# Kernel tuning notes

Hardware: AMD Instinct MI355X
Metric: run time of the kernel (lower is better)

Reference implementation:

```python
import jax, jax.numpy as jnp
import numpy as np

NEG_INF = -1e10  # matches torch's -10000000000.0 fill


def setup_inputs() -> dict:
    key = jax.random.key(0)
    k1, k2, k3, k4, k5, k6 = jax.random.split(key, 6)
    B, N, D_IN, D_HID, D_OUT = 8, 2048, 512, 512, 512
    H = jax.random.normal(k1, (B, N, D_IN), dtype=jnp.float32)
    bias = jax.random.normal(k2, (B, N, N), dtype=jnp.float32)
    mask = jax.random.randint(k3, (B, N, N), 0, 2, dtype=jnp.int32)
    s = 1.0 / np.sqrt(D_IN)
    Wq = jax.random.normal(k4, (D_IN, D_HID), dtype=jnp.float32) * s
    Wk = jax.random.normal(k5, (D_IN, D_HID), dtype=jnp.float32) * s
    Wv = jax.random.normal(k6, (D_IN, D_OUT), dtype=jnp.float32) * s
    return {"H": H, "bias": bias, "mask": mask, "Wq": Wq, "Wk": Wk, "Wv": Wv}


def reference(H, bias, mask, Wq, Wk, Wv):
    # Q,K: [B,N,d_hid], V: [B,N,d_out]
    Q = H @ Wq
    K = H @ Wk
    V = H @ Wv
    d = Q.shape[-1]
    scale = 1.0 / jnp.sqrt(jnp.asarray(d, dtype=Q.dtype))
    # scores: [B,N,N]; scale, add bias, then fill masked-out entries
    scores = jnp.einsum("bnd,bmd->bnm", Q, K) * scale + bias
    scores = jnp.where(mask == 0, jnp.asarray(NEG_INF, scores.dtype), scores)
    atn = jax.nn.softmax(scores, axis=-1)
    return jnp.einsum("bnm,bmo->bno", atn, V)
```

## Files before the change

kernel.cpp:

```cpp
#include <hip/hip_runtime.h>
#include <hip/hip_bf16.h>

typedef __attribute__((ext_vector_type(8))) short short8;
typedef __attribute__((ext_vector_type(4))) float floatx4;

#define NB 8
#define NN 2048
#define DD 512

__device__ __forceinline__ unsigned short f2bf(float f) {
  union { float f; unsigned int u; } v; v.f = f;
  unsigned int u = v.u;
  return (unsigned short)((u + 0x7fffu + ((u >> 16) & 1u)) >> 16);
}
__device__ __forceinline__ float bf2f(unsigned short s) {
  union { unsigned int u; float f; } v; v.u = ((unsigned int)s) << 16;
  return v.f;
}

typedef __attribute__((address_space(3))) unsigned short lds_us;
typedef __attribute__((address_space(1))) const unsigned short glb_us;

__device__ __forceinline__ void ld_lds16(const unsigned short* g, unsigned short* l) {
  __builtin_amdgcn_global_load_lds((glb_us*)g, (lds_us*)l, 16, 0, 0);
}

__global__ __launch_bounds__(256) void mha_cvtH(const float* __restrict__ H,
                                                unsigned short* __restrict__ Hb, int n8) {
  int i = blockIdx.x * 256 + threadIdx.x;
  if (i >= n8) return;
  const float4* src = (const float4*)H;
  float4 a = src[2 * i], b = src[2 * i + 1];
  short8 o;
  o[0] = (short)f2bf(a.x); o[1] = (short)f2bf(a.y); o[2] = (short)f2bf(a.z); o[3] = (short)f2bf(a.w);
  o[4] = (short)f2bf(b.x); o[5] = (short)f2bf(b.y); o[6] = (short)f2bf(b.z); o[7] = (short)f2bf(b.w);
  *(short8*)(Hb + 8 * i) = o;
}

__global__ __launch_bounds__(256) void mha_tW(const float* __restrict__ Wq, const float* __restrict__ Wk,
                                              const float* __restrict__ Wv,
                                              unsigned short* __restrict__ Wqt, unsigned short* __restrict__ Wkt,
                                              unsigned short* __restrict__ Wvt) {
  const float* W = (blockIdx.z == 0) ? Wq : (blockIdx.z == 1) ? Wk : Wv;
  unsigned short* Wt = (blockIdx.z == 0) ? Wqt : (blockIdx.z == 1) ? Wkt : Wvt;
  __shared__ float tile[32][33];
  int d0 = blockIdx.x * 32, k0 = blockIdx.y * 32;
  int t = threadIdx.x, r = t >> 3, c4 = (t & 7) * 4;
  float4 v = *(const float4*)(W + (size_t)(k0 + r) * DD + d0 + c4);
  tile[r][c4] = v.x; tile[r][c4 + 1] = v.y; tile[r][c4 + 2] = v.z; tile[r][c4 + 3] = v.w;
  __syncthreads();
  union { unsigned short s[4]; uint2 v; } u;
  u.s[0] = f2bf(tile[c4][r]);     u.s[1] = f2bf(tile[c4 + 1][r]);
  u.s[2] = f2bf(tile[c4 + 2][r]); u.s[3] = f2bf(tile[c4 + 3][r]);
  *(uint2*)(Wt + (size_t)(d0 + r) * DD + k0 + c4) = u.v;
}

__global__ __launch_bounds__(256) void mha_tV(const unsigned short* __restrict__ Vr,
                                              unsigned short* __restrict__ Vt) {
  int b = blockIdx.z;
  int d0 = blockIdx.x * 32, n0 = blockIdx.y * 32;
  __shared__ unsigned short tile[32][34];
  int t = threadIdx.x, r = t >> 3, c4 = (t & 7) * 4;
  union { uint2 v; unsigned short s[4]; } u;
  u.v = *(const uint2*)(Vr + ((size_t)b * NN + n0 + r) * DD + d0 + c4);
  tile[r][c4] = u.s[0]; tile[r][c4 + 1] = u.s[1]; tile[r][c4 + 2] = u.s[2]; tile[r][c4 + 3] = u.s[3];
  __syncthreads();
  union { unsigned short s[4]; uint2 v; } o;
  o.s[0] = tile[c4][r]; o.s[1] = tile[c4 + 1][r]; o.s[2] = tile[c4 + 2][r]; o.s[3] = tile[c4 + 3][r];
  *(uint2*)(Vt + ((size_t)b * DD + d0 + r) * NN + n0 + c4) = o.v;
}


__device__ __forceinline__ void stage_tile_async(const unsigned short* __restrict__ g, int ld,
                                                 unsigned short* s, int t) {
#pragma unroll
  for (int h = 0; h < 2; ++h) {
    int c = t + h * 256;
    int r = c >> 2, p = c & 3;
    int seg = (p - (r >> 1)) & 3;
    ld_lds16(g + (size_t)r * ld + seg * 8, s + c * 8);
  }
}

__device__ __forceinline__ void mfma_step(const unsigned short* As, const unsigned short* Bs,
                                          int wr, int wc, int quad, int lr, floatx4 acc[4][4]) {
  short8 a[4], b[4];
#pragma unroll
  for (int i = 0; i < 4; ++i) {
    int ra = wr * 64 + i * 16 + lr;
    int rb = wc * 64 + i * 16 + lr;
    a[i] = *(const short8*)(As + ra * 32 + ((quad + (ra >> 1)) & 3) * 8);
    b[i] = *(const short8*)(Bs + rb * 32 + ((quad + (rb >> 1)) & 3) * 8);
  }
#pragma unroll
  for (int i = 0; i < 4; ++i)
#pragma unroll
    for (int j = 0; j < 4; ++j)
      acc[i][j] = __builtin_amdgcn_mfma_f32_16x16x32_bf16(a[i], b[j], acc[i][j], 0, 0, 0);
}

__global__ __launch_bounds__(256) void mha_proj(const unsigned short* __restrict__ Hb,
                                                const unsigned short* __restrict__ Wqt,
                                                const unsigned short* __restrict__ Wkt,
                                                const unsigned short* __restrict__ Wvt,
                                                unsigned short* __restrict__ Qb,
                                                unsigned short* __restrict__ Kb,
                                                unsigned short* __restrict__ Vr) {
  const unsigned short* Wt = (blockIdx.z == 0) ? Wqt : (blockIdx.z == 1) ? Wkt : Wvt;
  unsigned short* dst = (blockIdx.z == 0) ? Qb : (blockIdx.z == 1) ? Kb : Vr;
  __shared__ unsigned short As[128 * 32], Bs[128 * 32];
  int t = threadIdx.x, wave = t >> 6, lane = t & 63, quad = lane >> 4, lr = lane & 15;
  int wr = wave >> 1, wc = wave & 1;
  int m0 = blockIdx.y * 128, n0 = blockIdx.x * 128;
  floatx4 acc[4][4] = {};
  for (int k0 = 0; k0 < DD; k0 += 32) {
    __syncthreads();
    stage_tile_async(Hb + (size_t)m0 * DD + k0, DD, As, t);
    stage_tile_async(Wt + (size_t)n0 * DD + k0, DD, Bs, t);
    __syncthreads();
    mfma_step(As, Bs, wr, wc, quad, lr, acc);
  }
#pragma unroll
  for (int i = 0; i < 4; ++i)
#pragma unroll
    for (int j = 0; j < 4; ++j)
#pragma unroll
      for (int r = 0; r < 4; ++r) {
        int row = m0 + wr * 64 + i * 16 + quad * 4 + r;
        int col = n0 + wc * 64 + j * 16 + lr;
        dst[(size_t)row * DD + col] = f2bf(acc[i][j][r]);
      }
}

__global__ __launch_bounds__(256) void mha_scores(const unsigned short* __restrict__ Qb,
                                                  const unsigned short* __restrict__ Kb,
                                                  const float* __restrict__ bias,
                                                  const int* __restrict__ mask,
                                                  unsigned short* __restrict__ E,
                                                  float* __restrict__ l) {
  int b = blockIdx.z;
  int i0 = blockIdx.y * 128;
  int j0 = blockIdx.x * 128;
  __shared__ unsigned short As[128 * 32], Bs[128 * 32];
  int t = threadIdx.x, wave = t >> 6, lane = t & 63, quad = lane >> 4, lr = lane & 15;
  int wr = wave >> 1, wc = wave & 1;
  const unsigned short* Q = Qb + (size_t)b * NN * DD;
  const unsigned short* K = Kb + (size_t)b * NN * DD;
  const float scale = 0.04419417382415922f;

  floatx4 acc[4][4] = {};
  for (int k0 = 0; k0 < DD; k0 += 32) {
    __syncthreads();
    stage_tile_async(Q + (size_t)i0 * DD + k0, DD, As, t);
    stage_tile_async(K + (size_t)j0 * DD + k0, DD, Bs, t);
    __syncthreads();
    mfma_step(As, Bs, wr, wc, quad, lr, acc);
  }

  float rs[4][4] = {};
#pragma unroll
  for (int i = 0; i < 4; ++i) {
    int row = i0 + wr * 64 + i * 16 + quad * 4;
#pragma unroll
    for (int j = 0; j < 4; ++j) {
      int col = j0 + wc * 64 + j * 16 + lr;
      size_t base = ((size_t)b * NN + row) * NN + col;
#pragma unroll
      for (int r = 0; r < 4; ++r) {
        size_t off = base + (size_t)r * NN;
        float bi = __builtin_nontemporal_load(&bias[off]);
        int mk = __builtin_nontemporal_load(&mask[off]);
        float s = acc[i][j][r] * scale + bi - 16.0f;
        float e = (mk != 0) ? __expf(s) : 0.0f;
        unsigned short eb = f2bf(e);
        E[off] = eb;
        rs[i][r] += bf2f(eb);
      }
    }
  }
#pragma unroll
  for (int i = 0; i < 4; ++i)
#pragma unroll
    for (int r = 0; r < 4; ++r) {
      float v = rs[i][r];
      v += __shfl_xor(v, 1);
      v += __shfl_xor(v, 2);
      v += __shfl_xor(v, 4);
      v += __shfl_xor(v, 8);
      if (lr == 0) {
        int row = i0 + wr * 64 + i * 16 + quad * 4 + r;
        atomicAdd(&l[b * NN + row], v);
      }
    }
}

__global__ __launch_bounds__(256) void mha_pv(const unsigned short* __restrict__ E,
                                              const unsigned short* __restrict__ Vt,
                                              const float* __restrict__ l,
                                              float* __restrict__ out) {
  int b = blockIdx.z;
  int i0 = blockIdx.y * 128;
  int c0 = blockIdx.x * 128;
  __shared__ unsigned short As[128 * 32], Bs[128 * 32];
  int t = threadIdx.x, wave = t >> 6, lane = t & 63, quad = lane >> 4, lr = lane & 15;
  int wr = wave >> 1, wc = wave & 1;
  const unsigned short* Eb = E + (size_t)b * NN * NN;
  const unsigned short* Vb = Vt + (size_t)b * DD * NN;
  floatx4 acc[4][4] = {};
  for (int k0 = 0; k0 < NN; k0 += 32) {
    __syncthreads();
    stage_tile_async(Eb + (size_t)i0 * NN + k0, NN, As, t);
    stage_tile_async(Vb + (size_t)c0 * NN + k0, NN, Bs, t);
    __syncthreads();
    mfma_step(As, Bs, wr, wc, quad, lr, acc);
  }
#pragma unroll
  for (int i = 0; i < 4; ++i)
#pragma unroll
    for (int r = 0; r < 4; ++r) {
      int row = i0 + wr * 64 + i * 16 + quad * 4 + r;
      float linv = 1.0f / l[b * NN + row];
#pragma unroll
      for (int j = 0; j < 4; ++j) {
        int col = c0 + wc * 64 + j * 16 + lr;
        __builtin_nontemporal_store(acc[i][j][r] * linv,
                                    &out[((size_t)b * NN + row) * DD + col]);
      }
    }
}

extern "C" void kernel_launch(void* const* d_in, const int* in_sizes, int n_in,
                              void* d_out, int out_size, void* d_ws, size_t ws_size,
                              hipStream_t stream) {
  const float* H = (const float*)d_in[0];
  const float* bias = (const float*)d_in[1];
  const int* mask = (const int*)d_in[2];
  const float* Wq = (const float*)d_in[3];
  const float* Wk = (const float*)d_in[4];
  const float* Wv = (const float*)d_in[5];
  float* out = (float*)d_out;
  char* ws = (char*)d_ws;

  const size_t SZ_QKV = (size_t)NB * NN * DD * 2;
  const size_t SZ_W = (size_t)DD * DD * 2;
  unsigned short* Qb = (unsigned short*)(ws);
  unsigned short* Kb = (unsigned short*)(ws + SZ_QKV);
  unsigned short* Vt = (unsigned short*)(ws + 2 * SZ_QKV);
  float* l = (float*)(ws + 3 * SZ_QKV);
  char* base2 = ws + 3 * SZ_QKV + (((size_t)NB * NN * 4 + 255) & ~255ULL);
  unsigned short* E = (unsigned short*)(base2);
  unsigned short* Hb = (unsigned short*)(base2);
  unsigned short* Wqt = (unsigned short*)(base2 + SZ_QKV);
  unsigned short* Wkt = (unsigned short*)(base2 + SZ_QKV + SZ_W);
  unsigned short* Wvt = (unsigned short*)(base2 + SZ_QKV + 2 * SZ_W);
  unsigned short* Vr = (unsigned short*)(base2 + SZ_QKV + 3 * SZ_W);

  hipMemsetAsync(l, 0, (size_t)NB * NN * 4, stream);
  mha_cvtH<<<dim3((NB * NN * DD / 8) / 256), 256, 0, stream>>>(H, Hb, NB * NN * DD / 8);
  mha_tW<<<dim3(DD / 32, DD / 32, 3), 256, 0, stream>>>(Wq, Wk, Wv, Wqt, Wkt, Wvt);
  mha_proj<<<dim3(DD / 128, NB * NN / 128, 3), 256, 0, stream>>>(Hb, Wqt, Wkt, Wvt, Qb, Kb, Vr);
  mha_tV<<<dim3(DD / 32, NN / 32, NB), 256, 0, stream>>>(Vr, Vt);
  mha_scores<<<dim3(NN / 128, NN / 128, NB), 256, 0, stream>>>(Qb, Kb, bias, mask, E, l);
  mha_pv<<<dim3(DD / 128, NN / 128, NB), 256, 0, stream>>>(E, Vt, l, out);
}
```

Before: 587.4 us.

## Fuse score and PV kernels into flash-style attention without materialized E

Replaces the separate scores kernel (which wrote a bf16 exp-score matrix E to global memory) and the PV kernel with one fused kernel. Each block handles 32 query rows for one batch, loops over key tiles, builds exp scores in LDS, and multiplies them by V directly. Row sums are reduced in shared memory, which removes the global atomics and the memset. This avoids writing and reading back the large E matrix. The cost is that each block now reloads K and V for every 32-row tile, and the tiles are smaller with fewer blocks (8x64).

```diff
diff --git a/kernel.cpp b/kernel.cpp
--- a/kernel.cpp
+++ b/kernel.cpp
@@ -132,100 +132,143 @@
       }
 }
 
-__global__ __launch_bounds__(256) void mha_scores(const unsigned short* __restrict__ Qb,
-                                                  const unsigned short* __restrict__ Kb,
-                                                  const float* __restrict__ bias,
-                                                  const int* __restrict__ mask,
-                                                  unsigned short* __restrict__ E,
-                                                  float* __restrict__ l) {
-  int b = blockIdx.z;
-  int i0 = blockIdx.y * 128;
-  int j0 = blockIdx.x * 128;
-  __shared__ unsigned short As[128 * 32], Bs[128 * 32];
+__global__ __launch_bounds__(256, 2) void mha_fused(const unsigned short* __restrict__ Qb,
+                                                    const unsigned short* __restrict__ Kb,
+                                                    const unsigned short* __restrict__ Vt,
+                                                    const float* __restrict__ bias,
+                                                    const int* __restrict__ mask,
+                                                    float* __restrict__ out) {
+  __shared__ unsigned short smem[40960];
+  unsigned short* Qs = smem;
+  unsigned short* Ks = smem + 4096;
+  unsigned short* Ps = smem + 20480;
+  unsigned short* Vs = smem + 24576;
+  float* ls = (float*)smem;
+
+  int b = blockIdx.x;
+  int i0 = blockIdx.y * 32;
   int t = threadIdx.x, wave = t >> 6, lane = t & 63, quad = lane >> 4, lr = lane & 15;
-  int wr = wave >> 1, wc = wave & 1;
-  const unsigned short* Q = Qb + (size_t)b * NN * DD;
-  const unsigned short* K = Kb + (size_t)b * NN * DD;
+  const unsigned short* Qg = Qb + ((size_t)b * NN + i0) * DD;
+  const unsigned short* Kg = Kb + (size_t)b * NN * DD;
+  const unsigned short* Vg = Vt + (size_t)b * DD * NN;
   const float scale = 0.04419417382415922f;
 
-  floatx4 acc[4][4] = {};
-  for (int k0 = 0; k0 < DD; k0 += 32) {
+  floatx4 acc[2][8] = {};
+  float rs[2][4] = {};
+
+  for (int jt = 0; jt < 16; ++jt) {
+    int j0 = jt * 128;
+    floatx4 sacc[2][2] = {};
+
+    for (int k0 = 0; k0 < DD; k0 += 128) {
+      __syncthreads();
+#pragma unroll
+      for (int h = 0; h < 2; ++h) {
+        int d = t + h * 256;
+        int s = d >> 7, w = d & 127, r = w >> 2, p = w & 3;
+        int l = (p - (r >> 1)) & 3;
+        ld_lds16(Qg + (size_t)r * DD + k0 + (s * 4 + l) * 8, Qs + d * 8);
+      }
+#pragma unroll
+      for (int h = 0; h < 8; ++h) {
+        int d = t + h * 256;
+        int s = d >> 9, w = d & 511, r = w >> 2, p = w & 3;
+        int l = (p - (r >> 1)) & 3;
+        ld_lds16(Kg + (size_t)(j0 + r) * DD + k0 + (s * 4 + l) * 8, Ks + d * 8);
+      }
+      __syncthreads();
+#pragma unroll
+      for (int ss = 0; ss < 4; ++ss) {
+        short8 a[2], bb[2];
+#pragma unroll
+        for (int i = 0; i < 2; ++i) {
+          int ra = i * 16 + lr;
+          a[i] = *(const short8*)(Qs + ss * 1024 + ra * 32 + ((quad + (ra >> 1)) & 3) * 8);
+        }
+#pragma unroll
+        for (int j = 0; j < 2; ++j) {
+          int rb = wave * 32 + j * 16 + lr;
+          bb[j] = *(const short8*)(Ks + ss * 4096 + rb * 32 + ((quad + (rb >> 1)) & 3) * 8);
+        }
+#pragma unroll
+        for (int i = 0; i < 2; ++i)
+#pragma unroll
+          for (int j = 0; j < 2; ++j)
+            sacc[i][j] = __builtin_amdgcn_mfma_f32_16x16x32_bf16(a[i], bb[j], sacc[i][j], 0, 0, 0);
+      }
+    }
+
+#pragma unroll
+    for (int i = 0; i < 2; ++i)
+#pragma unroll
+      for (int jj = 0; jj < 2; ++jj)
+#pragma unroll
+        for (int rr = 0; rr < 4; ++rr) {
+          int row_l = i * 16 + quad * 4 + rr;
+          int jloc = jj * 16 + lr;
+          size_t off = ((size_t)b * NN + i0 + row_l) * NN + (j0 + wave * 32 + jloc);
+          float bi = __builtin_nontemporal_load(&bias[off]);
+          int mk = __builtin_nontemporal_load(&mask[off]);
+          float s = sacc[i][jj][rr] * scale + bi - 16.0f;
+          float e = (mk != 0) ? __expf(s) : 0.0f;
+          unsigned short eb = f2bf(e);
+          Ps[wave * 1024 + row_l * 32 + (((jloc >> 3) + (row_l >> 1)) & 3) * 8 + (jloc & 7)] = eb;
+          rs[i][rr] += bf2f(eb);
+        }
     __syncthreads();
-    stage_tile_async(Q + (size_t)i0 * DD + k0, DD, As, t);
-    stage_tile_async(K + (size_t)j0 * DD + k0, DD, Bs, t);
-    __syncthreads();
-    mfma_step(As, Bs, wr, wc, quad, lr, acc);
-  }
-
-  float rs[4][4] = {};
-#pragma unroll
-  for (int i = 0; i < 4; ++i) {
-    int row = i0 + wr * 64 + i * 16 + quad * 4;
-#pragma unroll
-    for (int j = 0; j < 4; ++j) {
-      int col = j0 + wc * 64 + j * 16 + lr;
-      size_t base = ((size_t)b * NN + row) * NN + col;
-#pragma unroll
-      for (int r = 0; r < 4; ++r) {
-        size_t off = base + (size_t)r * NN;
-        float bi = __builtin_nontemporal_load(&bias[off]);
-        int mk = __builtin_nontemporal_load(&mask[off]);
-        float s = acc[i][j][r] * scale + bi - 16.0f;
-        float e = (mk != 0) ? __expf(s) : 0.0f;
-        unsigned short eb = f2bf(e);
-        E[off] = eb;
-        rs[i][r] += bf2f(eb);
+
+    for (int jk = 0; jk < 4; ++jk) {
+      if (jk) __syncthreads();
+#pragma unroll
+      for (int h = 0; h < 8; ++h) {
+        int d = t + h * 256;
+        int r = d >> 2, p = d & 3;
+        int l = (p - (r >> 1)) & 3;
+        ld_lds16(Vg + (size_t)r * NN + j0 + jk * 32 + l * 8, Vs + d * 8);
+      }
+      __syncthreads();
+      short8 a[2];
+#pragma unroll
+      for (int i = 0; i < 2; ++i) {
+        int ra = i * 16 + lr;
+        a[i] = *(const short8*)(Ps + jk * 1024 + ra * 32 + ((quad + (ra >> 1)) & 3) * 8);
+      }
+#pragma unroll
+      for (int jc = 0; jc < 8; ++jc) {
+        int rb = wave * 128 + jc * 16 + lr;
+        short8 bv = *(const short8*)(Vs + rb * 32 + ((quad + (rb >> 1)) & 3) * 8);
+        acc[0][jc] = __builtin_amdgcn_mfma_f32_16x16x32_bf16(a[0], bv, acc[0][jc], 0, 0, 0);
+        acc[1][jc] = __builtin_amdgcn_mfma_f32_16x16x32_bf16(a[1], bv, acc[1][jc], 0, 0, 0);
       }
     }
   }
-#pragma unroll
-  for (int i = 0; i < 4; ++i)
-#pragma unroll
-    for (int r = 0; r < 4; ++r) {
-      float v = rs[i][r];
+
+  __syncthreads();
+  if (t < 32) ls[t] = 0.0f;
+  __syncthreads();
+#pragma unroll
+  for (int i = 0; i < 2; ++i)
+#pragma unroll
+    for (int rr = 0; rr < 4; ++rr) {
+      float v = rs[i][rr];
       v += __shfl_xor(v, 1);
       v += __shfl_xor(v, 2);
       v += __shfl_xor(v, 4);
       v += __shfl_xor(v, 8);
-      if (lr == 0) {
-        int row = i0 + wr * 64 + i * 16 + quad * 4 + r;
-        atomicAdd(&l[b * NN + row], v);
-      }
+      if (lr == 0) atomicAdd(&ls[i * 16 + quad * 4 + rr], v);
     }
-}
-
-__global__ __launch_bounds__(256) void mha_pv(const unsigned short* __restrict__ E,
-                                              const unsigned short* __restrict__ Vt,
-                                              const float* __restrict__ l,
-                                              float* __restrict__ out) {
-  int b = blockIdx.z;
-  int i0 = blockIdx.y * 128;
-  int c0 = blockIdx.x * 128;
-  __shared__ unsigned short As[128 * 32], Bs[128 * 32];
-  int t = threadIdx.x, wave = t >> 6, lane = t & 63, quad = lane >> 4, lr = lane & 15;
-  int wr = wave >> 1, wc = wave & 1;
-  const unsigned short* Eb = E + (size_t)b * NN * NN;
-  const unsigned short* Vb = Vt + (size_t)b * DD * NN;
-  floatx4 acc[4][4] = {};
-  for (int k0 = 0; k0 < NN; k0 += 32) {
-    __syncthreads();
-    stage_tile_async(Eb + (size_t)i0 * NN + k0, NN, As, t);
-    stage_tile_async(Vb + (size_t)c0 * NN + k0, NN, Bs, t);
-    __syncthreads();
-    mfma_step(As, Bs, wr, wc, quad, lr, acc);
-  }
-#pragma unroll
-  for (int i = 0; i < 4; ++i)
-#pragma unroll
-    for (int r = 0; r < 4; ++r) {
-      int row = i0 + wr * 64 + i * 16 + quad * 4 + r;
-      float linv = 1.0f / l[b * NN + row];
-#pragma unroll
-      for (int j = 0; j < 4; ++j) {
-        int col = c0 + wc * 64 + j * 16 + lr;
-        __builtin_nontemporal_store(acc[i][j][r] * linv,
-                                    &out[((size_t)b * NN + row) * DD + col]);
-      }
+  __syncthreads();
+
+#pragma unroll
+  for (int i = 0; i < 2; ++i)
+#pragma unroll
+    for (int rr = 0; rr < 4; ++rr) {
+      int row_l = i * 16 + quad * 4 + rr;
+      float linv = 1.0f / ls[row_l];
+      size_t rowoff = ((size_t)b * NN + i0 + row_l) * DD + wave * 128;
+#pragma unroll
+      for (int jc = 0; jc < 8; ++jc)
+        __builtin_nontemporal_store(acc[i][jc][rr] * linv, &out[rowoff + jc * 16 + lr]);
     }
 }
 
@@ -246,20 +289,15 @@
   unsigned short* Qb = (unsigned short*)(ws);
   unsigned short* Kb = (unsigned short*)(ws + SZ_QKV);
   unsigned short* Vt = (unsigned short*)(ws + 2 * SZ_QKV);
-  float* l = (float*)(ws + 3 * SZ_QKV);
-  char* base2 = ws + 3 * SZ_QKV + (((size_t)NB * NN * 4 + 255) & ~255ULL);
-  unsigned short* E = (unsigned short*)(base2);
-  unsigned short* Hb = (unsigned short*)(base2);
-  unsigned short* Wqt = (unsigned short*)(base2 + SZ_QKV);
-  unsigned short* Wkt = (unsigned short*)(base2 + SZ_QKV + SZ_W);
-  unsigned short* Wvt = (unsigned short*)(base2 + SZ_QKV + 2 * SZ_W);
-  unsigned short* Vr = (unsigned short*)(base2 + SZ_QKV + 3 * SZ_W);
-
-  hipMemsetAsync(l, 0, (size_t)NB * NN * 4, stream);
+  unsigned short* Hb = (unsigned short*)(ws + 3 * SZ_QKV);
+  unsigned short* Wqt = (unsigned short*)(ws + 4 * SZ_QKV);
+  unsigned short* Wkt = (unsigned short*)(ws + 4 * SZ_QKV + SZ_W);
+  unsigned short* Wvt = (unsigned short*)(ws + 4 * SZ_QKV + 2 * SZ_W);
+  unsigned short* Vr = (unsigned short*)(ws + 4 * SZ_QKV + 3 * SZ_W);
+
   mha_cvtH<<<dim3((NB * NN * DD / 8) / 256), 256, 0, stream>>>(H, Hb, NB * NN * DD / 8);
   mha_tW<<<dim3(DD / 32, DD / 32, 3), 256, 0, stream>>>(Wq, Wk, Wv, Wqt, Wkt, Wvt);
   mha_proj<<<dim3(DD / 128, NB * NN / 128, 3), 256, 0, stream>>>(Hb, Wqt, Wkt, Wvt, Qb, Kb, Vr);
   mha_tV<<<dim3(DD / 32, NN / 32, NB), 256, 0, stream>>>(Vr, Vt);
-  mha_scores<<<dim3(NN / 128, NN / 128, NB), 256, 0, stream>>>(Qb, Kb, bias, mask, E, l);
-  mha_pv<<<dim3(DD / 128, NN / 128, NB), 256, 0, stream>>>(E, Vt, l, out);
-}
+  mha_fused<<<dim3(NB, NN / 32), 256, 0, stream>>>(Qb, Kb, Vt, bias, mask, out);
+}
```

New measurement: 662.0 us. 12.7% more time.

## Pre-pack bias and mask into bf16 and prefetch it into LDS during QK GEMM

Applied to the files above, without the earlier changes.

A new streaming kernel merges the fp32 bias and int32 mask into a single bf16 tensor, using -inf for masked entries. The scores kernel then pulls its 128x128 tile of that tensor into a swizzled LDS buffer with async global-to-LDS loads during the first half of the K loop. This hides the bias read behind the MFMA work and removes the uncoalesced per-element bias and mask loads from the epilogue. The exponentials are written back in place over the packed buffer. In exchange, the whole bias and mask tensor gets an extra full read plus a write and re-read, the scores kernel needs 32KB more LDS (which may lower occupancy), and bias is rounded to bf16.

```diff
diff --git a/kernel.cpp b/kernel.cpp
--- a/kernel.cpp
+++ b/kernel.cpp
@@ -3,6 +3,8 @@
 
 typedef __attribute__((ext_vector_type(8))) short short8;
 typedef __attribute__((ext_vector_type(4))) float floatx4;
+typedef __attribute__((ext_vector_type(4))) int intx4;
+typedef __attribute__((ext_vector_type(4))) unsigned short ushortx4;
 
 #define NB 8
 #define NN 2048
@@ -35,6 +37,21 @@
   o[0] = (short)f2bf(a.x); o[1] = (short)f2bf(a.y); o[2] = (short)f2bf(a.z); o[3] = (short)f2bf(a.w);
   o[4] = (short)f2bf(b.x); o[5] = (short)f2bf(b.y); o[6] = (short)f2bf(b.z); o[7] = (short)f2bf(b.w);
   *(short8*)(Hb + 8 * i) = o;
+}
+
+__global__ __launch_bounds__(256) void mha_prep(const floatx4* __restrict__ bias,
+                                                const intx4* __restrict__ mask,
+                                                ushortx4* __restrict__ bm) {
+  int i = blockIdx.x * 256 + threadIdx.x;
+  floatx4 bv = __builtin_nontemporal_load(&bias[i]);
+  intx4 mv = __builtin_nontemporal_load(&mask[i]);
+  const unsigned short NINF = 0xFF80;
+  ushortx4 o;
+  o.x = mv.x ? f2bf(bv.x) : NINF;
+  o.y = mv.y ? f2bf(bv.y) : NINF;
+  o.z = mv.z ? f2bf(bv.z) : NINF;
+  o.w = mv.w ? f2bf(bv.w) : NINF;
+  __builtin_nontemporal_store(o, &bm[i]);
 }
 
 __global__ __launch_bounds__(256) void mha_tW(const float* __restrict__ Wq, const float* __restrict__ Wk,
@@ -70,7 +87,6 @@
   *(uint2*)(Vt + ((size_t)b * DD + d0 + r) * NN + n0 + c4) = o.v;
 }
 
-
 __device__ __forceinline__ void stage_tile_async(const unsigned short* __restrict__ g, int ld,
                                                  unsigned short* s, int t) {
 #pragma unroll
@@ -134,25 +150,31 @@
 
 __global__ __launch_bounds__(256) void mha_scores(const unsigned short* __restrict__ Qb,
                                                   const unsigned short* __restrict__ Kb,
-                                                  const float* __restrict__ bias,
-                                                  const int* __restrict__ mask,
-                                                  unsigned short* __restrict__ E,
+                                                  unsigned short* __restrict__ bmE,
                                                   float* __restrict__ l) {
+  __shared__ unsigned short As[128 * 32], Bs[128 * 32], Bm[128 * 128];
   int b = blockIdx.z;
   int i0 = blockIdx.y * 128;
   int j0 = blockIdx.x * 128;
-  __shared__ unsigned short As[128 * 32], Bs[128 * 32];
   int t = threadIdx.x, wave = t >> 6, lane = t & 63, quad = lane >> 4, lr = lane & 15;
   int wr = wave >> 1, wc = wave & 1;
   const unsigned short* Q = Qb + (size_t)b * NN * DD;
   const unsigned short* K = Kb + (size_t)b * NN * DD;
+  unsigned short* bm = bmE + (size_t)b * NN * NN;
   const float scale = 0.04419417382415922f;
 
   floatx4 acc[4][4] = {};
-  for (int k0 = 0; k0 < DD; k0 += 32) {
+  for (int kidx = 0; kidx < 16; ++kidx) {
+    int k0 = kidx * 32;
     __syncthreads();
     stage_tile_async(Q + (size_t)i0 * DD + k0, DD, As, t);
     stage_tile_async(K + (size_t)j0 * DD + k0, DD, Bs, t);
+    if (kidx < 8) {
+      int c = kidx * 256 + t;
+      int row = c >> 4, phys = c & 15;
+      int s = (phys - row) & 15;
+      ld_lds16(bm + (size_t)(i0 + row) * NN + j0 + s * 8, Bm + c * 8);
+    }
     __syncthreads();
     mfma_step(As, Bs, wr, wc, quad, lr, acc);
   }
@@ -160,20 +182,18 @@
   float rs[4][4] = {};
 #pragma unroll
   for (int i = 0; i < 4; ++i) {
-    int row = i0 + wr * 64 + i * 16 + quad * 4;
 #pragma unroll
     for (int j = 0; j < 4; ++j) {
-      int col = j0 + wc * 64 + j * 16 + lr;
-      size_t base = ((size_t)b * NN + row) * NN + col;
 #pragma unroll
       for (int r = 0; r < 4; ++r) {
-        size_t off = base + (size_t)r * NN;
-        float bi = __builtin_nontemporal_load(&bias[off]);
-        int mk = __builtin_nontemporal_load(&mask[off]);
-        float s = acc[i][j][r] * scale + bi - 16.0f;
-        float e = (mk != 0) ? __expf(s) : 0.0f;
+        int row_l = wr * 64 + i * 16 + quad * 4 + r;
+        int col_l = wc * 64 + j * 16 + lr;
+        int sseg = col_l >> 3;
+        float bi = bf2f(Bm[(row_l * 16 + ((sseg + row_l) & 15)) * 8 + (col_l & 7)]);
+        float sv = acc[i][j][r] * scale + bi - 16.0f;
+        float e = __expf(sv);
         unsigned short eb = f2bf(e);
-        E[off] = eb;
+        __builtin_nontemporal_store(eb, &bm[(size_t)(i0 + row_l) * NN + j0 + col_l]);
         rs[i][r] += bf2f(eb);
       }
     }
@@ -248,18 +268,20 @@
   unsigned short* Vt = (unsigned short*)(ws + 2 * SZ_QKV);
   float* l = (float*)(ws + 3 * SZ_QKV);
   char* base2 = ws + 3 * SZ_QKV + (((size_t)NB * NN * 4 + 255) & ~255ULL);
-  unsigned short* E = (unsigned short*)(base2);
+  unsigned short* bmE = (unsigned short*)(base2);
   unsigned short* Hb = (unsigned short*)(base2);
   unsigned short* Wqt = (unsigned short*)(base2 + SZ_QKV);
   unsigned short* Wkt = (unsigned short*)(base2 + SZ_QKV + SZ_W);
   unsigned short* Wvt = (unsigned short*)(base2 + SZ_QKV + 2 * SZ_W);
   unsigned short* Vr = (unsigned short*)(base2 + SZ_QKV + 3 * SZ_W);
 
-  hipMemsetAsync(l, 0, (size_t)NB * NN * 4, stream);
+  (void)hipMemsetAsync(l, 0, (size_t)NB * NN * 4, stream);
   mha_cvtH<<<dim3((NB * NN * DD / 8) / 256), 256, 0, stream>>>(H, Hb, NB * NN * DD / 8);
   mha_tW<<<dim3(DD / 32, DD / 32, 3), 256, 0, stream>>>(Wq, Wk, Wv, Wqt, Wkt, Wvt);
   mha_proj<<<dim3(DD / 128, NB * NN / 128, 3), 256, 0, stream>>>(Hb, Wqt, Wkt, Wvt, Qb, Kb, Vr);
   mha_tV<<<dim3(DD / 32, NN / 32, NB), 256, 0, stream>>>(Vr, Vt);
-  mha_scores<<<dim3(NN / 128, NN / 128, NB), 256, 0, stream>>>(Qb, Kb, bias, mask, E, l);
-  mha_pv<<<dim3(DD / 128, NN / 128, NB), 256, 0, stream>>>(E, Vt, l, out);
-}
+  mha_prep<<<dim3((NB * NN * NN / 4) / 256), 256, 0, stream>>>((const floatx4*)bias,
+                                                               (const intx4*)mask, (ushortx4*)bmE);
+  mha_scores<<<dim3(NN / 128, NN / 128, NB), 256, 0, stream>>>(Qb, Kb, bmE, l);
+  mha_pv<<<dim3(DD / 128, NN / 128, NB), 256, 0, stream>>>(bmE, Vt, l, out);
+}
```

Result: faster. 494.0 us (-15.9%).
